# Kernel optimization log

Measured on AMD Instinct MI355X. Metric: run time of the kernel, lower is better.

The kernel has to match this reference:

```python
import jax, jax.numpy as jnp
import numpy as np

GROUPS = 32
EPS = 1e-5
HEADS = 8

def setup_inputs() -> dict:
    key = jax.random.key(0)
    ks = jax.random.split(key, 7)
    b, c, H, W = 16, 512, 32, 32
    x = jax.random.normal(ks[0], (b, c, H, W), dtype=jnp.float32)
    gn_scale = jax.random.normal(ks[1], (c,), dtype=jnp.float32) * 0.02 + 1.0
    gn_bias = jax.random.normal(ks[2], (c,), dtype=jnp.float32) * 0.02
    w_qkv = jax.random.normal(ks[3], (3 * c, c), dtype=jnp.float32) / np.sqrt(c)
    b_qkv = jax.random.normal(ks[4], (3 * c,), dtype=jnp.float32) * 0.01
    # original zero-initializes proj_out; use random weights for a non-trivial baseline
    w_proj = jax.random.normal(ks[5], (c, c), dtype=jnp.float32) / np.sqrt(c)
    b_proj = jax.random.normal(ks[6], (c,), dtype=jnp.float32) * 0.01
    return {"x": x, "gn_scale": gn_scale, "gn_bias": gn_bias,
            "w_qkv": w_qkv, "b_qkv": b_qkv, "w_proj": w_proj, "b_proj": b_proj}

def _group_norm(x, scale, bias):
    # x: [b, c, T]; normalize over (c//GROUPS, T) per group
    b, c, T = x.shape
    xg = x.reshape(b, GROUPS, (c // GROUPS) * T)
    mean = xg.mean(axis=-1, keepdims=True)
    var = xg.var(axis=-1, keepdims=True)
    xn = ((xg - mean) * jax.lax.rsqrt(var + EPS)).reshape(b, c, T)
    return xn * scale[None, :, None] + bias[None, :, None]

def reference(x, gn_scale, gn_bias, w_qkv, b_qkv, w_proj, b_proj):
    b, c, H, W = x.shape
    T = H * W
    xf = x.reshape(b, c, T)
    h = _group_norm(xf, gn_scale, gn_bias)
    qkv = jnp.einsum('oc,bct->bot', w_qkv, h) + b_qkv[None, :, None]  # [b, 3c, T]
    qkv = qkv.reshape(b * HEADS, 3 * (c // HEADS), T)
    ch = c // HEADS
    q, k, v = jnp.split(qkv, 3, axis=1)  # each [b*heads, ch, T]
    scale = 1.0 / np.sqrt(np.sqrt(ch))
    weight = jnp.einsum('bct,bcs->bts', q * scale, k * scale)  # [b*heads, T, T]
    weight = jax.nn.softmax(weight.astype(jnp.float32), axis=-1).astype(qkv.dtype)
    r = jnp.einsum('bts,bcs->bct', weight, v)  # [b*heads, ch, T]
    r = r.reshape(b, c, T)
    out = jnp.einsum('oc,bct->bot', w_proj, r) + b_proj[None, :, None]
    return (xf + out).reshape(b, c, H, W)
```

## Files before the change

### kernel.cpp

```cpp
#include <hip/hip_runtime.h>
#include <stdint.h>
#include <stddef.h>

#define NB 16
#define NC 512
#define NT 1024
#define NHEAD 8
#define NOC 1536

typedef float f32x4 __attribute__((ext_vector_type(4)));
typedef short s16x8 __attribute__((ext_vector_type(8)));
typedef short s16x4 __attribute__((ext_vector_type(4)));
typedef unsigned int u32x2 __attribute__((ext_vector_type(2)));

#define AS1 __attribute__((address_space(1)))
#define AS3 __attribute__((address_space(3)))

static __device__ __forceinline__ unsigned short f2bf(float f) {
  union { float fv; unsigned int u; } v; v.fv = f;
  return (unsigned short)((v.u + 0x7fffu + ((v.u >> 16) & 1u)) >> 16);
}

static __device__ __forceinline__ unsigned int cvtpk(float lo, float hi) {
  unsigned int r;
  asm("v_cvt_pk_bf16_f32 %0, %1, %2" : "=v"(r) : "v"(lo), "v"(hi));
  return r;
}

static __device__ __forceinline__ float exp2_hw(float x) {
  float r;
  asm("v_exp_f32 %0, %1" : "=v"(r) : "v"(x));
  return r;
}

__global__ void k_convert(const float* __restrict__ wq, const float* __restrict__ wp,
                          unsigned short* __restrict__ wqb, unsigned short* __restrict__ wpb) {
  int i = blockIdx.x * 256 + threadIdx.x;
  int step = gridDim.x * 256;
  for (int idx = i; idx < NOC * NC; idx += step) wqb[idx] = f2bf(wq[idx]);
  for (int idx = i; idx < NC * NC; idx += step) wpb[idx] = f2bf(wp[idx]);
}

__global__ __launch_bounds__(256) void k_gnstats(const float* __restrict__ x,
    const float* __restrict__ gsc, const float* __restrict__ gbi,
    float* __restrict__ affA, float* __restrict__ affB) {
  int b = blockIdx.x >> 5, g = blockIdx.x & 31;
  const f32x4* p4 = (const f32x4*)(x + (size_t)(b * NC + g * 16) * NT);
  float s = 0.f, ss = 0.f;
  for (int i = threadIdx.x; i < 4096; i += 256) {
    f32x4 v = p4[i];
    s += v[0] + v[1] + v[2] + v[3];
    ss += v[0] * v[0] + v[1] * v[1] + v[2] * v[2] + v[3] * v[3];
  }
#pragma unroll
  for (int off = 32; off > 0; off >>= 1) { s += __shfl_down(s, off); ss += __shfl_down(ss, off); }
  __shared__ float red[4][2];
  if ((threadIdx.x & 63) == 0) { red[threadIdx.x >> 6][0] = s; red[threadIdx.x >> 6][1] = ss; }
  __syncthreads();
  if (threadIdx.x < 16) {
    float st = red[0][0] + red[1][0] + red[2][0] + red[3][0];
    float sst = red[0][1] + red[1][1] + red[2][1] + red[3][1];
    float mean = st * (1.f / 16384.f);
    float var = sst * (1.f / 16384.f) - mean * mean;
    float rstd = rsqrtf(var + 1e-5f);
    int c = g * 16 + threadIdx.x;
    float a = rstd * gsc[c];
    affA[b * NC + c] = a;
    affB[b * NC + c] = gbi[c] - mean * a;
  }
}

__global__ __launch_bounds__(256) void k_norm_t(const float* __restrict__ x,
    const float* __restrict__ affA, const float* __restrict__ affB,
    unsigned short* __restrict__ xt) {
  __shared__ float sm[64][65];
  int bx = blockIdx.x;
  int tt = bx & 15, ct = (bx >> 4) & 7, b = bx >> 7;
  int c0 = ct * 64, t0 = tt * 64;
  int tid = threadIdx.x;
#pragma unroll
  for (int it = 0; it < 4; it++) {
    int row = (tid >> 4) + it * 16;
    int col = (tid & 15) * 4;
    int c = c0 + row;
    f32x4 v = *(const f32x4*)(x + (size_t)(b * NC + c) * NT + t0 + col);
    float a = affA[b * NC + c], bb = affB[b * NC + c];
    sm[row][col + 0] = v[0] * a + bb;
    sm[row][col + 1] = v[1] * a + bb;
    sm[row][col + 2] = v[2] * a + bb;
    sm[row][col + 3] = v[3] * a + bb;
  }
  __syncthreads();
#pragma unroll
  for (int it = 0; it < 2; it++) {
    int t = (tid >> 3) + it * 32;
    int cb = (tid & 7) * 8;
    s16x8 o;
#pragma unroll
    for (int j = 0; j < 8; j++) o[j] = (short)f2bf(sm[cb + j][t]);
    *(s16x8*)(xt + (size_t)(b * NT + t0 + t) * NC + c0 + cb) = o;
  }
}

__global__ __launch_bounds__(256) void k_qkv(const unsigned short* __restrict__ wqb,
    const unsigned short* __restrict__ xt, const float* __restrict__ bqkv,
    unsigned short* __restrict__ qt, unsigned short* __restrict__ ktb,
    unsigned short* __restrict__ vvb) {
  __shared__ char Al[8192];
  __shared__ char Bl[8192];
  __shared__ char Tr[4][8192];
  int n0 = blockIdx.x * 128;
  int m0 = blockIdx.y * 128;
  int b = blockIdx.z;
  int tid = threadIdx.x, lane = tid & 63, wid = tid >> 6;
  int wr = wid >> 1, wc = wid & 1;
  int arow = lane >> 2, acol = (lane & 3) * 8;
  f32x4 acc[4][4] = {};
  for (int ks = 0; ks < 16; ks++) {
    int k0 = ks * 32;
    __syncthreads();
#pragma unroll
    for (int cc = 0; cc < 2; cc++) {
      int ci = wid * 2 + cc;
      const unsigned short* ga = wqb + (size_t)(m0 + ci * 16 + arow) * NC + k0 + acol;
      __builtin_amdgcn_global_load_lds((const AS1 unsigned int*)ga,
                                       (AS3 unsigned int*)(Al + ci * 1024), 16, 0, 0);
      const unsigned short* gb = xt + (size_t)(b * NT + n0 + ci * 16 + arow) * NC + k0 + acol;
      __builtin_amdgcn_global_load_lds((const AS1 unsigned int*)gb,
                                       (AS3 unsigned int*)(Bl + ci * 1024), 16, 0, 0);
    }
    __syncthreads();
    s16x8 af[4], bfv[4];
#pragma unroll
    for (int mi = 0; mi < 4; mi++)
      af[mi] = *(const s16x8*)(Al + ((wr * 64 + mi * 16 + (lane & 15)) * 32 + (lane >> 4) * 8) * 2);
#pragma unroll
    for (int ni = 0; ni < 4; ni++)
      bfv[ni] = *(const s16x8*)(Bl + ((wc * 64 + ni * 16 + (lane & 15)) * 32 + (lane >> 4) * 8) * 2);
#pragma unroll
    for (int mi = 0; mi < 4; mi++)
#pragma unroll
      for (int ni = 0; ni < 4; ni++)
        acc[mi][ni] = __builtin_amdgcn_mfma_f32_16x16x32_bf16(af[mi], bfv[ni], acc[mi][ni], 0, 0, 0);
  }
  char* tr = (char*)Tr[wid];
  int o064 = m0 + wr * 64;
  int blk = (o064 >> 6) % 3;
  int head = o064 / 192;
  int bh = b * NHEAD + head;
  int n0w = n0 + wc * 64;
  const float scale = 0.42466090014400953f;
  if (blk < 2) {
#pragma unroll
    for (int mi = 0; mi < 4; mi++) {
      int o_loc = mi * 16 + (lane >> 4) * 4;
      float b0 = bqkv[o064 + o_loc + 0], b1 = bqkv[o064 + o_loc + 1];
      float b2 = bqkv[o064 + o_loc + 2], b3 = bqkv[o064 + o_loc + 3];
#pragma unroll
      for (int ni = 0; ni < 4; ni++) {
        int t_loc = ni * 16 + (lane & 15);
        s16x4 pk;
        pk[0] = (short)f2bf((acc[mi][ni][0] + b0) * scale);
        pk[1] = (short)f2bf((acc[mi][ni][1] + b1) * scale);
        pk[2] = (short)f2bf((acc[mi][ni][2] + b2) * scale);
        pk[3] = (short)f2bf((acc[mi][ni][3] + b3) * scale);
        *(s16x4*)(tr + t_loc * 128 + ((o_loc * 2) ^ ((t_loc & 7) << 4))) = pk;
      }
    }
    unsigned short* outp = (blk == 0) ? qt : ktb;
#pragma unroll
    for (int pass = 0; pass < 8; pass++) {
      int t = pass * 8 + (lane >> 3);
      int cb = (lane & 7) * 16;
      s16x8 v = *(const s16x8*)(tr + t * 128 + (cb ^ ((t & 7) << 4)));
      *(s16x8*)(outp + (size_t)(bh * NT + n0w + t) * 64 + (cb >> 1)) = v;
    }
  } else {
#pragma unroll
    for (int mi = 0; mi < 4; mi++) {
#pragma unroll
      for (int ni = 0; ni < 4; ni++) {
        int t_loc = ni * 16 + (lane & 15);
#pragma unroll
        for (int r = 0; r < 4; r++) {
          int o_loc = mi * 16 + (lane >> 4) * 4 + r;
          *(unsigned short*)(tr + o_loc * 128 + t_loc * 2) =
              f2bf(acc[mi][ni][r] + bqkv[o064 + o_loc]);
        }
      }
    }
#pragma unroll
    for (int pass = 0; pass < 8; pass++) {
      int o = pass * 8 + (lane >> 3);
      int tb = (lane & 7) * 16;
      s16x8 v = *(const s16x8*)(tr + o * 128 + tb);
      *(s16x8*)(vvb + (size_t)(bh * 64 + o) * NT + n0w + (tb >> 1)) = v;
    }
  }
}

__global__ __launch_bounds__(512, 4) void k_attn(const unsigned short* __restrict__ qt,
    const unsigned short* __restrict__ ktb, const unsigned short* __restrict__ vvb,
    unsigned short* __restrict__ rt) {
  __shared__ char Kl[8192];
  __shared__ char Vl[8192];
  __shared__ char Pl[8][4096];
  int qt0 = blockIdx.x * 256;
  int bh = blockIdx.y;
  int b = bh >> 3, head = bh & 7;
  int tid = threadIdx.x, lane = tid & 63, wid = tid >> 6;
  int hi = lane >> 4, lo = lane & 15;
  int q0 = qt0 + wid * 32;
  s16x8 aq[2][2];
#pragma unroll
  for (int mi = 0; mi < 2; mi++)
#pragma unroll
    for (int ko = 0; ko < 2; ko++)
      aq[mi][ko] = *(const s16x8*)(qt + (size_t)(bh * NT + q0 + mi * 16 + lo) * 64 +
                                   ko * 32 + hi * 8);
  f32x4 oacc[2][4] = {};
  float mrun[2] = {-1e30f, -1e30f}, lrun[2] = {0.f, 0.f};
  char* pl = (char*)Pl[wid];
  int srow = (wid << 3) + (lane >> 3);
  int soff = ((lane & 7) << 4) ^ ((srow & 7) << 4);
  const char* kb = (const char*)ktb + ((size_t)bh * NT + srow) * 128 + soff;
  const char* vb = (const char*)vvb + ((size_t)(bh * 64 + srow)) * 2048 + soff;
  for (int kv = 0; kv < 16; kv++) {
    __syncthreads();
    __builtin_amdgcn_global_load_lds((const AS1 unsigned int*)(kb + (size_t)kv * 64 * 128),
                                     (AS3 unsigned int*)(Kl + (wid << 10)), 16, 0, 0);
    __builtin_amdgcn_global_load_lds((const AS1 unsigned int*)(vb + (size_t)kv * 128),
                                     (AS3 unsigned int*)(Vl + (wid << 10)), 16, 0, 0);
    __syncthreads();
    f32x4 sc[2][4] = {};
#pragma unroll
    for (int ni = 0; ni < 4; ni++) {
      int tkr = ni * 16 + lo;
#pragma unroll
      for (int ko = 0; ko < 2; ko++) {
        s16x8 kf = *(const s16x8*)(Kl + tkr * 128 + ((ko * 64 + hi * 16) ^ ((tkr & 7) << 4)));
        sc[0][ni] = __builtin_amdgcn_mfma_f32_16x16x32_bf16(kf, aq[0][ko], sc[0][ni], 0, 0, 0);
        sc[1][ni] = __builtin_amdgcn_mfma_f32_16x16x32_bf16(kf, aq[1][ko], sc[1][ni], 0, 0, 0);
      }
    }
#pragma unroll
    for (int mi = 0; mi < 2; mi++) {
      float a0 = fmaxf(fmaxf(sc[mi][0][0], sc[mi][0][1]), fmaxf(sc[mi][0][2], sc[mi][0][3]));
      float a1 = fmaxf(fmaxf(sc[mi][1][0], sc[mi][1][1]), fmaxf(sc[mi][1][2], sc[mi][1][3]));
      float a2 = fmaxf(fmaxf(sc[mi][2][0], sc[mi][2][1]), fmaxf(sc[mi][2][2], sc[mi][2][3]));
      float a3 = fmaxf(fmaxf(sc[mi][3][0], sc[mi][3][1]), fmaxf(sc[mi][3][2], sc[mi][3][3]));
      float tm = fmaxf(fmaxf(a0, a1), fmaxf(a2, a3));
      tm = fmaxf(tm, __shfl_xor(tm, 16));
      tm = fmaxf(tm, __shfl_xor(tm, 32));
      int resc = __any(tm > mrun[mi] + 8.f);
      float mnew = mrun[mi], fac = 1.f;
      if (resc) {
        mnew = fmaxf(mrun[mi], tm);
        fac = exp2_hw(mrun[mi] - mnew);
        mrun[mi] = mnew;
      }
      float ps = 0.f;
#pragma unroll
      for (int ni = 0; ni < 4; ni++)
#pragma unroll
        for (int r = 0; r < 4; r++) {
          float p = exp2_hw(sc[mi][ni][r] - mnew);
          sc[mi][ni][r] = p;
          ps += p;
        }
      ps += __shfl_xor(ps, 16);
      ps += __shfl_xor(ps, 32);
      lrun[mi] = (resc ? lrun[mi] * fac : lrun[mi]) + ps;
      int qrow = mi * 16 + lo;
#pragma unroll
      for (int ni = 0; ni < 4; ni++) {
        u32x2 w;
        w[0] = cvtpk(sc[mi][ni][0], sc[mi][ni][1]);
        w[1] = cvtpk(sc[mi][ni][2], sc[mi][ni][3]);
        *(u32x2*)(pl + (qrow * 128 + ((ni * 32 + hi * 8) ^ ((qrow & 7) << 4)))) = w;
      }
      if (resc) {
#pragma unroll
        for (int dm = 0; dm < 4; dm++)
#pragma unroll
          for (int r = 0; r < 4; r++) oacc[mi][dm][r] *= fac;
      }
    }
#pragma unroll
    for (int kt = 0; kt < 2; kt++) {
      s16x8 pa[2];
#pragma unroll
      for (int mi = 0; mi < 2; mi++) {
        int qrow = mi * 16 + lo;
        pa[mi] = *(const s16x8*)(pl + (qrow * 128 + ((kt * 64 + hi * 16) ^ ((qrow & 7) << 4))));
      }
#pragma unroll
      for (int dm = 0; dm < 4; dm++) {
        int dr = dm * 16 + lo;
        s16x8 av = *(const s16x8*)(Vl + dr * 128 + ((kt * 64 + hi * 16) ^ ((dr & 7) << 4)));
        oacc[0][dm] = __builtin_amdgcn_mfma_f32_16x16x32_bf16(av, pa[0], oacc[0][dm], 0, 0, 0);
        oacc[1][dm] = __builtin_amdgcn_mfma_f32_16x16x32_bf16(av, pa[1], oacc[1][dm], 0, 0, 0);
      }
    }
  }
#pragma unroll
  for (int mi = 0; mi < 2; mi++) {
    float inv = 1.f / lrun[mi];
    int q = q0 + mi * 16 + lo;
#pragma unroll
    for (int dm = 0; dm < 4; dm++) {
      u32x2 w;
      w[0] = cvtpk(oacc[mi][dm][0] * inv, oacc[mi][dm][1] * inv);
      w[1] = cvtpk(oacc[mi][dm][2] * inv, oacc[mi][dm][3] * inv);
      *(u32x2*)(rt + (size_t)(b * NT + q) * NC + head * 64 + dm * 16 + hi * 4) = w;
    }
  }
}

__global__ __launch_bounds__(256) void k_proj(const unsigned short* __restrict__ wpb,
    const unsigned short* __restrict__ rt, const float* __restrict__ bproj,
    const float* __restrict__ x, float* __restrict__ out) {
  __shared__ char Al[8192];
  __shared__ char Bl[8192];
  int n0 = blockIdx.x * 128;
  int m0 = blockIdx.y * 128;
  int b = blockIdx.z;
  int tid = threadIdx.x, lane = tid & 63, wid = tid >> 6;
  int wr = wid >> 1, wc = wid & 1;
  int arow = lane >> 2, acol = (lane & 3) * 8;
  f32x4 acc[4][4] = {};
  for (int ks = 0; ks < 16; ks++) {
    int k0 = ks * 32;
    __syncthreads();
#pragma unroll
    for (int cc = 0; cc < 2; cc++) {
      int ci = wid * 2 + cc;
      const unsigned short* ga = wpb + (size_t)(m0 + ci * 16 + arow) * NC + k0 + acol;
      __builtin_amdgcn_global_load_lds((const AS1 unsigned int*)ga,
                                       (AS3 unsigned int*)(Al + ci * 1024), 16, 0, 0);
      const unsigned short* gb = rt + (size_t)(b * NT + n0 + ci * 16 + arow) * NC + k0 + acol;
      __builtin_amdgcn_global_load_lds((const AS1 unsigned int*)gb,
                                       (AS3 unsigned int*)(Bl + ci * 1024), 16, 0, 0);
    }
    __syncthreads();
    s16x8 af[4], bfv[4];
#pragma unroll
    for (int mi = 0; mi < 4; mi++)
      af[mi] = *(const s16x8*)(Al + ((wr * 64 + mi * 16 + (lane & 15)) * 32 + (lane >> 4) * 8) * 2);
#pragma unroll
    for (int ni = 0; ni < 4; ni++)
      bfv[ni] = *(const s16x8*)(Bl + ((wc * 64 + ni * 16 + (lane & 15)) * 32 + (lane >> 4) * 8) * 2);
#pragma unroll
    for (int mi = 0; mi < 4; mi++)
#pragma unroll
      for (int ni = 0; ni < 4; ni++)
        acc[mi][ni] = __builtin_amdgcn_mfma_f32_16x16x32_bf16(af[mi], bfv[ni], acc[mi][ni], 0, 0, 0);
  }
#pragma unroll
  for (int mi = 0; mi < 4; mi++) {
    int o_base = m0 + wr * 64 + mi * 16 + (lane >> 4) * 4;
#pragma unroll
    for (int r = 0; r < 4; r++) {
      int o = o_base + r;
      float bp = bproj[o];
#pragma unroll
      for (int ni = 0; ni < 4; ni++) {
        int t = n0 + wc * 64 + ni * 16 + (lane & 15);
        size_t idx = (size_t)(b * NC + o) * NT + t;
        out[idx] = acc[mi][ni][r] + bp + x[idx];
      }
    }
  }
}

extern "C" void kernel_launch(void* const* d_in, const int* in_sizes, int n_in,
                              void* d_out, int out_size, void* d_ws, size_t ws_size,
                              hipStream_t stream) {
  const float* x   = (const float*)d_in[0];
  const float* gsc = (const float*)d_in[1];
  const float* gbi = (const float*)d_in[2];
  const float* wq  = (const float*)d_in[3];
  const float* bq  = (const float*)d_in[4];
  const float* wp  = (const float*)d_in[5];
  const float* bp  = (const float*)d_in[6];
  float* out = (float*)d_out;
  char* ws = (char*)d_ws;

  float* affA = (float*)ws;
  float* affB = affA + NB * NC;
  unsigned short* wqb = (unsigned short*)(ws + 65536);
  unsigned short* wpb = wqb + (size_t)NOC * NC;
  unsigned short* xt  = (unsigned short*)(ws + 2162688);
  unsigned short* qt  = xt + (size_t)NB * NT * NC;
  unsigned short* ktb = qt + (size_t)128 * NT * 64;
  unsigned short* vvb = ktb + (size_t)128 * NT * 64;
  unsigned short* rt  = vvb + (size_t)128 * NT * 64;

  k_convert<<<dim3(1024), 256, 0, stream>>>(wq, wp, wqb, wpb);
  k_gnstats<<<dim3(512), 256, 0, stream>>>(x, gsc, gbi, affA, affB);
  k_norm_t<<<dim3(2048), 256, 0, stream>>>(x, affA, affB, xt);
  k_qkv<<<dim3(8, 12, 16), 256, 0, stream>>>(wqb, xt, bq, qt, ktb, vvb);
  k_attn<<<dim3(4, 128), 512, 0, stream>>>(qt, ktb, vvb, rt);
  k_proj<<<dim3(8, 4, 16), 256, 0, stream>>>(wpb, rt, bp, x, out);
}
```

Before: 138.4 us.

## Double-buffer K/V tiles in attention and compute row sums via MFMA

Double-buffers the K and V tiles in LDS so the async global-to-LDS load of the next tile is issued before computing on the current one, with explicit vmcnt waits and raw barriers in place of two __syncthreads per iteration. The softmax denominator is no longer built from scalar sums and cross-lane shuffles; it comes from an extra MFMA of the bf16 probabilities against a ones vector. This hides load latency and removes shuffle work, at the cost of twice the K/V LDS, which may lower occupancy. The denominator now sums bf16-rounded probabilities, which matches the numerator more closely.

```diff
diff --git a/kernel.cpp b/kernel.cpp
--- a/kernel.cpp
+++ b/kernel.cpp
@@ -202,8 +202,8 @@
 __global__ __launch_bounds__(512, 4) void k_attn(const unsigned short* __restrict__ qt,
     const unsigned short* __restrict__ ktb, const unsigned short* __restrict__ vvb,
     unsigned short* __restrict__ rt) {
-  __shared__ char Kl[8192];
-  __shared__ char Vl[8192];
+  __shared__ char Kl[2][8192];
+  __shared__ char Vl[2][8192];
   __shared__ char Pl[8][4096];
   int qt0 = blockIdx.x * 256;
   int bh = blockIdx.y;
@@ -219,26 +219,40 @@
       aq[mi][ko] = *(const s16x8*)(qt + (size_t)(bh * NT + q0 + mi * 16 + lo) * 64 +
                                    ko * 32 + hi * 8);
   f32x4 oacc[2][4] = {};
-  float mrun[2] = {-1e30f, -1e30f}, lrun[2] = {0.f, 0.f};
+  f32x4 lacc[2] = {};
+  float mrun[2] = {-1e30f, -1e30f};
+  s16x8 ones;
+#pragma unroll
+  for (int j = 0; j < 8; j++) ones[j] = (short)0x3F80;
   char* pl = (char*)Pl[wid];
   int srow = (wid << 3) + (lane >> 3);
   int soff = ((lane & 7) << 4) ^ ((srow & 7) << 4);
   const char* kb = (const char*)ktb + ((size_t)bh * NT + srow) * 128 + soff;
   const char* vb = (const char*)vvb + ((size_t)(bh * 64 + srow)) * 2048 + soff;
+  __builtin_amdgcn_global_load_lds((const AS1 unsigned int*)kb,
+                                   (AS3 unsigned int*)(Kl[0] + (wid << 10)), 16, 0, 0);
+  __builtin_amdgcn_global_load_lds((const AS1 unsigned int*)vb,
+                                   (AS3 unsigned int*)(Vl[0] + (wid << 10)), 16, 0, 0);
   for (int kv = 0; kv < 16; kv++) {
-    __syncthreads();
-    __builtin_amdgcn_global_load_lds((const AS1 unsigned int*)(kb + (size_t)kv * 64 * 128),
-                                     (AS3 unsigned int*)(Kl + (wid << 10)), 16, 0, 0);
-    __builtin_amdgcn_global_load_lds((const AS1 unsigned int*)(vb + (size_t)kv * 128),
-                                     (AS3 unsigned int*)(Vl + (wid << 10)), 16, 0, 0);
-    __syncthreads();
+    int cur = kv & 1;
+    if (kv < 15) {
+      __builtin_amdgcn_global_load_lds((const AS1 unsigned int*)(kb + (size_t)(kv + 1) * 8192),
+                                       (AS3 unsigned int*)(Kl[cur ^ 1] + (wid << 10)), 16, 0, 0);
+      __builtin_amdgcn_global_load_lds((const AS1 unsigned int*)(vb + (size_t)(kv + 1) * 128),
+                                       (AS3 unsigned int*)(Vl[cur ^ 1] + (wid << 10)), 16, 0, 0);
+      asm volatile("s_waitcnt vmcnt(2)" ::: "memory");
+    } else {
+      asm volatile("s_waitcnt vmcnt(0)" ::: "memory");
+    }
+    __builtin_amdgcn_s_barrier();
+    __builtin_amdgcn_sched_barrier(0);
     f32x4 sc[2][4] = {};
 #pragma unroll
     for (int ni = 0; ni < 4; ni++) {
       int tkr = ni * 16 + lo;
 #pragma unroll
       for (int ko = 0; ko < 2; ko++) {
-        s16x8 kf = *(const s16x8*)(Kl + tkr * 128 + ((ko * 64 + hi * 16) ^ ((tkr & 7) << 4)));
+        s16x8 kf = *(const s16x8*)(Kl[cur] + tkr * 128 + ((ko * 64 + hi * 16) ^ ((tkr & 7) << 4)));
         sc[0][ni] = __builtin_amdgcn_mfma_f32_16x16x32_bf16(kf, aq[0][ko], sc[0][ni], 0, 0, 0);
         sc[1][ni] = __builtin_amdgcn_mfma_f32_16x16x32_bf16(kf, aq[1][ko], sc[1][ni], 0, 0, 0);
       }
@@ -253,24 +267,22 @@
       tm = fmaxf(tm, __shfl_xor(tm, 16));
       tm = fmaxf(tm, __shfl_xor(tm, 32));
       int resc = __any(tm > mrun[mi] + 8.f);
-      float mnew = mrun[mi], fac = 1.f;
+      float mnew = mrun[mi];
       if (resc) {
         mnew = fmaxf(mrun[mi], tm);
-        fac = exp2_hw(mrun[mi] - mnew);
+        float fac = exp2_hw(mrun[mi] - mnew);
         mrun[mi] = mnew;
-      }
-      float ps = 0.f;
+#pragma unroll
+        for (int dm = 0; dm < 4; dm++)
+#pragma unroll
+          for (int r = 0; r < 4; r++) oacc[mi][dm][r] *= fac;
+#pragma unroll
+        for (int r = 0; r < 4; r++) lacc[mi][r] *= fac;
+      }
 #pragma unroll
       for (int ni = 0; ni < 4; ni++)
 #pragma unroll
-        for (int r = 0; r < 4; r++) {
-          float p = exp2_hw(sc[mi][ni][r] - mnew);
-          sc[mi][ni][r] = p;
-          ps += p;
-        }
-      ps += __shfl_xor(ps, 16);
-      ps += __shfl_xor(ps, 32);
-      lrun[mi] = (resc ? lrun[mi] * fac : lrun[mi]) + ps;
+        for (int r = 0; r < 4; r++) sc[mi][ni][r] = exp2_hw(sc[mi][ni][r] - mnew);
       int qrow = mi * 16 + lo;
 #pragma unroll
       for (int ni = 0; ni < 4; ni++) {
@@ -279,12 +291,6 @@
         w[1] = cvtpk(sc[mi][ni][2], sc[mi][ni][3]);
         *(u32x2*)(pl + (qrow * 128 + ((ni * 32 + hi * 8) ^ ((qrow & 7) << 4)))) = w;
       }
-      if (resc) {
-#pragma unroll
-        for (int dm = 0; dm < 4; dm++)
-#pragma unroll
-          for (int r = 0; r < 4; r++) oacc[mi][dm][r] *= fac;
-      }
     }
 #pragma unroll
     for (int kt = 0; kt < 2; kt++) {
@@ -297,15 +303,18 @@
 #pragma unroll
       for (int dm = 0; dm < 4; dm++) {
         int dr = dm * 16 + lo;
-        s16x8 av = *(const s16x8*)(Vl + dr * 128 + ((kt * 64 + hi * 16) ^ ((dr & 7) << 4)));
+        s16x8 av = *(const s16x8*)(Vl[cur] + dr * 128 + ((kt * 64 + hi * 16) ^ ((dr & 7) << 4)));
         oacc[0][dm] = __builtin_amdgcn_mfma_f32_16x16x32_bf16(av, pa[0], oacc[0][dm], 0, 0, 0);
         oacc[1][dm] = __builtin_amdgcn_mfma_f32_16x16x32_bf16(av, pa[1], oacc[1][dm], 0, 0, 0);
       }
-    }
+      lacc[0] = __builtin_amdgcn_mfma_f32_16x16x32_bf16(ones, pa[0], lacc[0], 0, 0, 0);
+      lacc[1] = __builtin_amdgcn_mfma_f32_16x16x32_bf16(ones, pa[1], lacc[1], 0, 0, 0);
+    }
+    __builtin_amdgcn_s_barrier();
   }
 #pragma unroll
   for (int mi = 0; mi < 2; mi++) {
-    float inv = 1.f / lrun[mi];
+    float inv = 1.f / lacc[mi][0];
     int q = q0 + mi * 16 + lo;
 #pragma unroll
     for (int dm = 0; dm < 4; dm++) {
```

Result: faster. 135.7 us (-2.0%).
